# Performance work log

Measured on AMD Instinct MI355X. Metric: run time of the kernel, lower is better.

The kernel has to match this reference:

```python
import jax, jax.numpy as jnp
import numpy as np

# Static network layout: inputs occupy columns [0, I), hidden [I, N-O), outputs [N-O, N)
B = 16384  # batch size
N = 1024   # total neurons
I = 128    # input neurons
O = 64     # output neurons
REFRACTORY = 0.9


def _activate(x, act_ids):
    """Vectorized per-neuron heterogeneous activation.
    act_ids: 0=relu, 1=tanh, 2=sigmoid, 3=identity.
    Replaces the original serial per-neuron getattr dispatch loop."""
    r = jax.nn.relu(x)
    t = jnp.tanh(x)
    s = jax.nn.sigmoid(x)
    return jnp.select([act_ids == 0, act_ids == 1, act_ids == 2], [r, t, s], x)


def setup_inputs() -> dict:
    key = jax.random.key(0)
    k0, k1, k2, k3, k4 = jax.random.split(key, 5)
    return {
        "prev_states": jax.random.normal(k0, (B, N), jnp.float32),
        "input_values": jax.random.normal(k1, (B, I), jnp.float32),
        "weight_matrix": jax.random.normal(k2, (N, N), jnp.float32) * 0.05,
        "biases": jax.random.normal(k3, (N,), jnp.float32) * 0.1,
        "act_ids": jax.random.randint(k4, (N,), 0, 4, dtype=jnp.int32),
    }


def reference(prev_states, input_values, weight_matrix, biases, act_ids):
    # _apply_refractory_factor on hidden cols + _assign_input_values on input cols
    states = jnp.concatenate(
        [input_values,
         prev_states[:, I:N - O] * REFRACTORY,
         prev_states[:, N - O:]],
        axis=1)  # [B, N]
    # total_input = states @ W + b
    total = states @ weight_matrix + biases  # [B, N]
    # activation applied to every non-input neuron; input neurons keep their state
    activated = _activate(total, act_ids[None, :])  # [B, N]
    new_states = jnp.concatenate([states[:, :I], activated[:, I:]], axis=1)
    # return output-layer slice
    return new_states[:, N - O:]
```

## Files before the change

kernel.cpp:

```cpp
#include <hip/hip_runtime.h>
#include <math.h>

#define BATCH 16384
#define NN    1024
#define NI    128
#define NO    64
#define REFR  0.9f

typedef float  f32x4  __attribute__((ext_vector_type(4)));
typedef __bf16 bf16x8 __attribute__((ext_vector_type(8)));

__global__ __launch_bounds__(256) void pack_w_kernel(const float* __restrict__ W,
                                                     __bf16* __restrict__ wsB) {
    int idx = blockIdx.x * 256 + threadIdx.x;
    int k = idx >> 6;
    int n = idx & 63;
    float v = W[(size_t)k * NN + (NN - NO) + n];
    int kc = k >> 5;
    if (kc >= 4 && kc < 30) v *= REFR;
    int kk = k & 31;
    int r3 = kk >> 3;
    int j  = kk & 7;
    int tn = n >> 4;
    int l  = r3 * 16 + (n & 15);
    wsB[(size_t)(((kc * 4 + tn) * 64 + l) * 8 + j)] = (__bf16)v;
}

__device__ inline float activate(float x, int id) {
    if (id == 0) return fmaxf(x, 0.0f);
    if (id == 1) return tanhf(x);
    if (id == 2) return 1.0f / (1.0f + __expf(-x));
    return x;
}

__global__ __launch_bounds__(256, 4) void fused_rnn_kernel(
    const float* __restrict__ prev,
    const float* __restrict__ inp,
    const __bf16* __restrict__ wsB,
    const float* __restrict__ bias,
    const int*  __restrict__ act,
    float* __restrict__ out)
{
    const int lane = threadIdx.x & 63;
    const int wv   = threadIdx.x >> 6;
    const int m    = lane & 15;
    const int q    = lane >> 4;
    const int row0 = blockIdx.x * 16;
    const int rowA = row0 + m;

    const float* prow = prev + (size_t)rowA * NN;
    const float* irow = inp  + (size_t)rowA * NI;
    const bf16x8* Bf  = (const bf16x8*)wsB;

    f32x4 acc[4];
    acc[0] = (f32x4){0.f, 0.f, 0.f, 0.f};
    acc[1] = acc[0]; acc[2] = acc[0]; acc[3] = acc[0];

    const int qo = q * 8;

#pragma unroll
    for (int i = 0; i < 8; ++i) {
        const int kc = wv * 8 + i;
        const float* srcRow = (kc < 4) ? irow : prow;

        const float4* p = (const float4*)(srcRow + kc * 32 + qo);
        float4 f0 = p[0];
        float4 f1 = p[1];
        bf16x8 a;
        a[0] = (__bf16)f0.x; a[1] = (__bf16)f0.y;
        a[2] = (__bf16)f0.z; a[3] = (__bf16)f0.w;
        a[4] = (__bf16)f1.x; a[5] = (__bf16)f1.y;
        a[6] = (__bf16)f1.z; a[7] = (__bf16)f1.w;

        const bf16x8* bp = Bf + (size_t)kc * 256 + lane;
        acc[0] = __builtin_amdgcn_mfma_f32_16x16x32_bf16(a, bp[0],   acc[0], 0, 0, 0);
        acc[1] = __builtin_amdgcn_mfma_f32_16x16x32_bf16(a, bp[64],  acc[1], 0, 0, 0);
        acc[2] = __builtin_amdgcn_mfma_f32_16x16x32_bf16(a, bp[128], acc[2], 0, 0, 0);
        acc[3] = __builtin_amdgcn_mfma_f32_16x16x32_bf16(a, bp[192], acc[3], 0, 0, 0);
    }

    __shared__ float red[4][16][68];
#pragma unroll
    for (int t = 0; t < 4; ++t) {
#pragma unroll
        for (int r = 0; r < 4; ++r) {
            red[wv][q * 4 + r][t * 16 + m] = acc[t][r];
        }
    }
    __syncthreads();

    const int orow = threadIdx.x >> 4;
    const int oc   = (threadIdx.x & 15) * 4;

    f32x4 s;
    {
        const f32x4* p0 = (const f32x4*)&red[0][orow][oc];
        const f32x4* p1 = (const f32x4*)&red[1][orow][oc];
        const f32x4* p2 = (const f32x4*)&red[2][orow][oc];
        const f32x4* p3 = (const f32x4*)&red[3][orow][oc];
        s = *p0 + *p1 + *p2 + *p3;
    }

    const float* bo = bias + (NN - NO);
    const int*   ao = act  + (NN - NO);
    f32x4 o;
#pragma unroll
    for (int c = 0; c < 4; ++c) {
        o[c] = activate(s[c] + bo[oc + c], ao[oc + c]);
    }
    *(f32x4*)(out + (size_t)(row0 + orow) * NO + oc) = o;
}

extern "C" void kernel_launch(void* const* d_in, const int* in_sizes, int n_in,
                              void* d_out, int out_size, void* d_ws, size_t ws_size,
                              hipStream_t stream) {
    const float* prev = (const float*)d_in[0];
    const float* inp  = (const float*)d_in[1];
    const float* W    = (const float*)d_in[2];
    const float* bias = (const float*)d_in[3];
    const int*   act  = (const int*)  d_in[4];
    float* out = (float*)d_out;
    __bf16* wsB = (__bf16*)d_ws;

    pack_w_kernel<<<256, 256, 0, stream>>>(W, wsB);

    fused_rnn_kernel<<<BATCH / 16, 256, 0, stream>>>(prev, inp, wsB, bias, act, out);
}
```

Baseline: 116.3 us.

## Process 32 rows per block with prefetched nontemporal loads and shared B fragments

Each block now handles two 16-row tiles, so every B fragment loaded from the packed weight buffer feeds two MFMAs. All activation loads are issued up front as nontemporal vector loads, half before the loop and half inside it, to keep more memory requests in flight. The launch bound drops to 2 waves per SIMD to make room for the extra registers, at the risk of lower occupancy and fewer blocks (512) to spread across the GPU.

Result: no change. 118.0 us (+1.4%).

```diff
diff --git a/kernel.cpp b/kernel.cpp
--- a/kernel.cpp
+++ b/kernel.cpp
@@ -33,7 +33,7 @@
     return x;
 }
 
-__global__ __launch_bounds__(256, 4) void fused_rnn_kernel(
+__global__ __launch_bounds__(256, 2) void fused_rnn_kernel(
     const float* __restrict__ prev,
     const float* __restrict__ inp,
     const __bf16* __restrict__ wsB,
@@ -45,46 +45,77 @@
     const int wv   = threadIdx.x >> 6;
     const int m    = lane & 15;
     const int q    = lane >> 4;
-    const int row0 = blockIdx.x * 16;
-    const int rowA = row0 + m;
+    const int row0 = blockIdx.x * 32;
 
-    const float* prow = prev + (size_t)rowA * NN;
-    const float* irow = inp  + (size_t)rowA * NI;
-    const bf16x8* Bf  = (const bf16x8*)wsB;
+    const float* prow0 = prev + (size_t)(row0 + m) * NN;
+    const float* prow1 = prev + (size_t)(row0 + 16 + m) * NN;
+    const float* irow0 = inp  + (size_t)(row0 + m) * NI;
+    const float* irow1 = inp  + (size_t)(row0 + 16 + m) * NI;
+    const bf16x8* Bf   = (const bf16x8*)wsB;
+    const int qo = q * 8;
 
-    f32x4 acc[4];
-    acc[0] = (f32x4){0.f, 0.f, 0.f, 0.f};
-    acc[1] = acc[0]; acc[2] = acc[0]; acc[3] = acc[0];
+    f32x4 acc0[4], acc1[4];
+#pragma unroll
+    for (int t = 0; t < 4; ++t) {
+        acc0[t] = (f32x4){0.f, 0.f, 0.f, 0.f};
+        acc1[t] = acc0[t];
+    }
 
-    const int qo = q * 8;
+    f32x4 A0a[8], A0b[8], A1a[8], A1b[8];
+
+#define LOADC(i) {                                                           \
+        const int kc_ = wv * 8 + (i);                                        \
+        const float* s0_ = (kc_ < 4) ? irow0 : prow0;                        \
+        const float* s1_ = (kc_ < 4) ? irow1 : prow1;                        \
+        const f32x4* p0_ = (const f32x4*)(s0_ + kc_ * 32 + qo);              \
+        const f32x4* p1_ = (const f32x4*)(s1_ + kc_ * 32 + qo);              \
+        A0a[i] = __builtin_nontemporal_load(p0_);                            \
+        A0b[i] = __builtin_nontemporal_load(p0_ + 1);                        \
+        A1a[i] = __builtin_nontemporal_load(p1_);                            \
+        A1b[i] = __builtin_nontemporal_load(p1_ + 1);                        \
+    }
+
+#pragma unroll
+    for (int i = 0; i < 4; ++i) LOADC(i)
 
 #pragma unroll
     for (int i = 0; i < 8; ++i) {
+        if (i < 4) LOADC(i + 4)
         const int kc = wv * 8 + i;
-        const float* srcRow = (kc < 4) ? irow : prow;
 
-        const float4* p = (const float4*)(srcRow + kc * 32 + qo);
-        float4 f0 = p[0];
-        float4 f1 = p[1];
-        bf16x8 a;
-        a[0] = (__bf16)f0.x; a[1] = (__bf16)f0.y;
-        a[2] = (__bf16)f0.z; a[3] = (__bf16)f0.w;
-        a[4] = (__bf16)f1.x; a[5] = (__bf16)f1.y;
-        a[6] = (__bf16)f1.z; a[7] = (__bf16)f1.w;
+        bf16x8 a0, a1;
+#pragma unroll
+        for (int e = 0; e < 4; ++e) {
+            a0[e]     = (__bf16)A0a[i][e];
+            a0[e + 4] = (__bf16)A0b[i][e];
+            a1[e]     = (__bf16)A1a[i][e];
+            a1[e + 4] = (__bf16)A1b[i][e];
+        }
 
         const bf16x8* bp = Bf + (size_t)kc * 256 + lane;
-        acc[0] = __builtin_amdgcn_mfma_f32_16x16x32_bf16(a, bp[0],   acc[0], 0, 0, 0);
-        acc[1] = __builtin_amdgcn_mfma_f32_16x16x32_bf16(a, bp[64],  acc[1], 0, 0, 0);
-        acc[2] = __builtin_amdgcn_mfma_f32_16x16x32_bf16(a, bp[128], acc[2], 0, 0, 0);
-        acc[3] = __builtin_amdgcn_mfma_f32_16x16x32_bf16(a, bp[192], acc[3], 0, 0, 0);
+        bf16x8 b0 = bp[0];
+        bf16x8 b1 = bp[64];
+        bf16x8 b2 = bp[128];
+        bf16x8 b3 = bp[192];
+
+        acc0[0] = __builtin_amdgcn_mfma_f32_16x16x32_bf16(a0, b0, acc0[0], 0, 0, 0);
+        acc1[0] = __builtin_amdgcn_mfma_f32_16x16x32_bf16(a1, b0, acc1[0], 0, 0, 0);
+        acc0[1] = __builtin_amdgcn_mfma_f32_16x16x32_bf16(a0, b1, acc0[1], 0, 0, 0);
+        acc1[1] = __builtin_amdgcn_mfma_f32_16x16x32_bf16(a1, b1, acc1[1], 0, 0, 0);
+        acc0[2] = __builtin_amdgcn_mfma_f32_16x16x32_bf16(a0, b2, acc0[2], 0, 0, 0);
+        acc1[2] = __builtin_amdgcn_mfma_f32_16x16x32_bf16(a1, b2, acc1[2], 0, 0, 0);
+        acc0[3] = __builtin_amdgcn_mfma_f32_16x16x32_bf16(a0, b3, acc0[3], 0, 0, 0);
+        acc1[3] = __builtin_amdgcn_mfma_f32_16x16x32_bf16(a1, b3, acc1[3], 0, 0, 0);
     }
+#undef LOADC
 
-    __shared__ float red[4][16][68];
+    __shared__ __align__(16) float red[4][2][16][68];
 #pragma unroll
     for (int t = 0; t < 4; ++t) {
 #pragma unroll
         for (int r = 0; r < 4; ++r) {
-            red[wv][q * 4 + r][t * 16 + m] = acc[t][r];
+            red[wv][0][q * 4 + r][t * 16 + m] = acc0[t][r];
+            red[wv][1][q * 4 + r][t * 16 + m] = acc1[t][r];
         }
     }
     __syncthreads();
@@ -92,23 +123,26 @@
     const int orow = threadIdx.x >> 4;
     const int oc   = (threadIdx.x & 15) * 4;
 
-    f32x4 s;
-    {
-        const f32x4* p0 = (const f32x4*)&red[0][orow][oc];
-        const f32x4* p1 = (const f32x4*)&red[1][orow][oc];
-        const f32x4* p2 = (const f32x4*)&red[2][orow][oc];
-        const f32x4* p3 = (const f32x4*)&red[3][orow][oc];
-        s = *p0 + *p1 + *p2 + *p3;
+    f32x4 s0 = *(const f32x4*)&red[0][0][orow][oc];
+    f32x4 s1 = *(const f32x4*)&red[0][1][orow][oc];
+#pragma unroll
+    for (int w = 1; w < 4; ++w) {
+        s0 += *(const f32x4*)&red[w][0][orow][oc];
+        s1 += *(const f32x4*)&red[w][1][orow][oc];
     }
 
     const float* bo = bias + (NN - NO);
     const int*   ao = act  + (NN - NO);
-    f32x4 o;
+    f32x4 o0, o1;
 #pragma unroll
     for (int c = 0; c < 4; ++c) {
-        o[c] = activate(s[c] + bo[oc + c], ao[oc + c]);
+        const float b  = bo[oc + c];
+        const int   id = ao[oc + c];
+        o0[c] = activate(s0[c] + b, id);
+        o1[c] = activate(s1[c] + b, id);
     }
-    *(f32x4*)(out + (size_t)(row0 + orow) * NO + oc) = o;
+    *(f32x4*)(out + (size_t)(row0 + orow) * NO + oc)      = o0;
+    *(f32x4*)(out + (size_t)(row0 + 16 + orow) * NO + oc) = o1;
 }
 
 extern "C" void kernel_launch(void* const* d_in, const int* in_sizes, int n_in,
@@ -124,5 +158,5 @@
 
     pack_w_kernel<<<256, 256, 0, stream>>>(W, wsB);
 
-    fused_rnn_kernel<<<BATCH / 16, 256, 0, stream>>>(prev, inp, wsB, bias, act, out);
+    fused_rnn_kernel<<<BATCH / 32, 256, 0, stream>>>(prev, inp, wsB, bias, act, out);
 }
```
